# Kernel tuning notes

Measured on AMD Instinct MI355X. Metric: run time of the kernel, lower is better.

## Reference

```python
import jax, jax.numpy as jnp
import numpy as np

NUM_MIXTURES = 10
DIM_INPUT = 512
DIM_FEATURES = 512
SEQ_LEN = 512
BATCH = 16
NUM_CHAR = 1024
DIM_CONTEXT = 256


def setup_inputs() -> dict:
    key = jax.random.key(0)
    ks = jax.random.split(key, 6)
    inputs = jax.random.normal(ks[0], (SEQ_LEN, BATCH, DIM_INPUT), dtype=jnp.float32)
    context_vectors = jax.random.normal(ks[1], (NUM_CHAR, BATCH, DIM_CONTEXT), dtype=jnp.float32)
    init_means = jnp.zeros((BATCH, NUM_MIXTURES), dtype=jnp.float32)
    # StackedLinearLayers params: 2 layers, leaky_relu between, out dim = 3*K
    s1 = 1.0 / np.sqrt(DIM_INPUT)
    s2 = 1.0 / np.sqrt(DIM_FEATURES)
    W1 = jax.random.uniform(ks[2], (DIM_INPUT, DIM_FEATURES), jnp.float32, -s1, s1)
    b1 = jax.random.uniform(ks[3], (DIM_FEATURES,), jnp.float32, -s1, s1)
    W2 = jax.random.uniform(ks[4], (DIM_FEATURES, 3 * NUM_MIXTURES), jnp.float32, -s2, s2)
    b2 = jax.random.uniform(ks[5], (3 * NUM_MIXTURES,), jnp.float32, -s2, s2)
    return dict(inputs=inputs, context_vectors=context_vectors, init_means=init_means,
                W1=W1, b1=b1, W2=W2, b2=b2, extra_chars=0)


def reference(inputs, context_vectors, init_means, W1, b1, W2, b2, extra_chars):
    K = NUM_MIXTURES
    seq_len, batch, _ = inputs.shape
    num_char = context_vectors.shape[0]
    total_char = num_char + extra_chars

    # StackedLinearLayers: leaky_relu MLP, last layer linear -> (S, B, 3K)
    h = jax.nn.leaky_relu(inputs @ W1 + b1, negative_slope=0.01)
    outs = h @ W2 + b2
    outs = jax.nn.softplus(outs)  # pos_fun = softplus

    delta_means, vars_, weights = jnp.split(outs, 3, axis=2)  # each (S, B, K)
    delta_means = delta_means / 25.0
    vars_ = jnp.clip(vars_, 0.01, 100.0)
    means = jnp.cumsum(delta_means, axis=0) + init_means[None, :, :]  # (S, B, K)

    cidxs = jnp.arange(total_char, dtype=jnp.float32)  # (T,)
    # dists: (S, B, K, T)
    dists = -((means[..., None] - cidxs) ** 2) * vars_[..., None]
    # attn_weights = exp(logsumexp over mixtures)
    attn_weights = jnp.exp(
        jax.scipy.special.logsumexp(jnp.log(weights)[..., None] + dists, axis=2)
    )  # (S, B, T)

    # attended contexts: (S, B, D)
    attn_contexts = jnp.einsum('sbc,cbd->sbd', attn_weights[:, :, :num_char], context_vectors)
    return attn_contexts, attn_weights, means, vars_, weights
```

## Files before the change

kernel.cpp:

```cpp
#include <hip/hip_runtime.h>
#include <math.h>

#define S_LEN 512
#define BATCH 16
#define DIN   512
#define DF    512
#define NMIX  10
#define NCHAR 1024
#define DCTX  256
#define M_ROWS (S_LEN*BATCH)

#define OFF_CTXOUT 0
#define OFF_ATTN   (S_LEN*BATCH*DCTX)
#define OFF_MEANS  (OFF_ATTN + S_LEN*BATCH*NCHAR)
#define OFF_VARS   (OFF_MEANS + S_LEN*BATCH*NMIX)
#define OFF_WTS    (OFF_VARS  + S_LEN*BATCH*NMIX)

#define WS_XH    0
#define WS_W1H   (8u<<20)
#define WS_W2T   (9u<<20)
#define WS_HH    (10u<<20)
#define WS_CTXH  (18u<<20)
#define WS_ATTNH (26u<<20)
#define WS_BOUND (44u<<20)

#define NX4     1048576
#define NW14    65536
#define NCTX4   1048576
#define CVT4    (NX4 + NW14 + NCTX4)
#define CVT_BLOCKS (CVT4/256)
#define W2T_BLOCKS 64

typedef float    f32x16 __attribute__((ext_vector_type(16)));
typedef _Float16 f16x8  __attribute__((ext_vector_type(8)));

__device__ __forceinline__ unsigned short f2h(float x) {
    union { _Float16 h; unsigned short u; } cv;
    cv.h = (_Float16)x;
    return cv.u;
}
__device__ __forceinline__ ushort4 cvt4(float4 v) {
    ushort4 o; o.x = f2h(v.x); o.y = f2h(v.y); o.z = f2h(v.z); o.w = f2h(v.w);
    return o;
}

__global__ __launch_bounds__(256) void convert_kernel(
    const float* __restrict__ X, const float* __restrict__ W1,
    const float* __restrict__ ctx, const float* __restrict__ W2,
    unsigned short* __restrict__ Xh, unsigned short* __restrict__ W1h,
    unsigned short* __restrict__ ctxh, float* __restrict__ W2T,
    unsigned int* __restrict__ bound)
{
    const int bid = blockIdx.x;
    if (bid < CVT_BLOCKS) {
        const int i4 = bid*256 + threadIdx.x;
        if (i4 < NX4) {
            ((ushort4*)Xh)[i4] = cvt4(((const float4*)X)[i4]);
        } else if (i4 < NX4 + NW14) {
            ((ushort4*)W1h)[i4 - NX4] = cvt4(((const float4*)W1)[i4 - NX4]);
        } else {
            const int j = i4 - NX4 - NW14;
            ((ushort4*)ctxh)[j] = cvt4(((const float4*)ctx)[j]);
        }
    } else if (bid < CVT_BLOCKS + W2T_BLOCKS) {
        const int idx = (bid - CVT_BLOCKS)*256 + threadIdx.x;
        if (idx < 512*32) {
            const int j = idx >> 9, k = idx & 511;
            W2T[idx] = (j < 30) ? W2[k*30 + j] : 0.f;
        }
    } else {
        if (threadIdx.x < BATCH) bound[threadIdx.x] = 0u;
    }
}

__global__ __launch_bounds__(256) void gemm1_kernel(
    const unsigned short* __restrict__ Xh, const unsigned short* __restrict__ W1h,
    const float* __restrict__ b1, unsigned short* __restrict__ Hh)
{
    __shared__ __align__(16) unsigned short As[64*72];
    __shared__ __align__(16) unsigned short Bs[64*72];
    const int row0 = (blockIdx.x >> 3) * 64;
    const int n0   = (blockIdx.x & 7)  * 64;
    const int tid  = threadIdx.x;
    const int lane = tid & 63, w = tid >> 6;
    const int wr = (w >> 1) * 32, wc = (w & 1) * 32;
    const int m  = lane & 31,  g  = lane >> 5;
    const int sa = tid >> 2,   ka = (tid & 3) * 16;
    const int kb = tid & 63,   wb = tid >> 6;

    f32x16 acc = {};

    for (int kt = 0; kt < DIN; kt += 64) {
        uint4 av0 = *(const uint4*)(Xh  + (size_t)(row0+sa)*DIN + kt + ka);
        uint4 av1 = *(const uint4*)(Xh  + (size_t)(row0+sa)*DIN + kt + ka + 8);
        uint4 bv0 = *(const uint4*)(W1h + (size_t)(kt+kb)*DF + n0 + wb*16);
        uint4 bv1 = *(const uint4*)(W1h + (size_t)(kt+kb)*DF + n0 + wb*16 + 8);
        __syncthreads();
        *(uint4*)(As + sa*72 + ka)     = av0;
        *(uint4*)(As + sa*72 + ka + 8) = av1;
        {
            union { uint4 u; unsigned short s[8]; } p0, p1;
            p0.u = bv0; p1.u = bv1;
            #pragma unroll
            for (int i = 0; i < 8; i++) Bs[(wb*16 + i)*72 + kb]     = p0.s[i];
            #pragma unroll
            for (int i = 0; i < 8; i++) Bs[(wb*16 + 8 + i)*72 + kb] = p1.s[i];
        }
        __syncthreads();
        #pragma unroll
        for (int ks = 0; ks < 64; ks += 16) {
            f16x8 af = *(const f16x8*)(As + (wr+m)*72 + ks + g*8);
            f16x8 bf = *(const f16x8*)(Bs + (wc+m)*72 + ks + g*8);
            acc = __builtin_amdgcn_mfma_f32_32x32x16_f16(af, bf, acc, 0, 0, 0);
        }
    }
    const int ncol = n0 + wc + m;
    const float bb = b1[ncol];
    #pragma unroll
    for (int r = 0; r < 16; r++) {
        const int rowloc = (r & 3) + 8*(r >> 2) + 4*g;
        const int row = row0 + wr + rowloc;
        float v = acc[r] + bb;
        v = v > 0.f ? v : 0.01f * v;
        Hh[(size_t)row*DF + ncol] = f2h(v);
    }
}

__global__ __launch_bounds__(256) void gemm2_kernel(
    const unsigned short* __restrict__ Hh, const float* __restrict__ W2T,
    const float* __restrict__ b2,
    float* __restrict__ dmeans, float* __restrict__ dvars, float* __restrict__ dwts)
{
    __shared__ __align__(16) unsigned short Hs[32*520];
    const int tid = threadIdx.x;
    const int r0  = blockIdx.x * 32;
    {
        const uint4* src = (const uint4*)(Hh + (size_t)r0*DF);
        #pragma unroll
        for (int i = 0; i < 8; i++) {
            int u   = tid + i*256;
            int row = u >> 6;
            int col = (u & 63) * 8;
            *(uint4*)(Hs + row*520 + col) = src[u];
        }
    }
    __syncthreads();

    const int r  = tid & 31;
    const int j0 = tid >> 5;
    const unsigned short* hrow = Hs + r*520;
    float acc[4] = {0.f, 0.f, 0.f, 0.f};

    for (int k0 = 0; k0 < DF; k0 += 8) {
        union { uint4 u; _Float16 h[8]; } hv;
        hv.u = *(const uint4*)(hrow + k0);
        float wv[4][8];
        #pragma unroll
        for (int q = 0; q < 4; q++) {
            *(float4*)(wv[q])     = *(const float4*)(W2T + (size_t)(j0 + q*8)*DF + k0);
            *(float4*)(wv[q] + 4) = *(const float4*)(W2T + (size_t)(j0 + q*8)*DF + k0 + 4);
        }
        #pragma unroll
        for (int i = 0; i < 8; i++) {
            float hf = (float)hv.h[i];
            acc[0] = fmaf(hf, wv[0][i], acc[0]);
            acc[1] = fmaf(hf, wv[1][i], acc[1]);
            acc[2] = fmaf(hf, wv[2][i], acc[2]);
            acc[3] = fmaf(hf, wv[3][i], acc[3]);
        }
    }
    const int row = r0 + r;
    #pragma unroll
    for (int q = 0; q < 4; q++) {
        const int j = j0 + q*8;
        if (j >= 30) continue;
        float dot = acc[q] + b2[j];
        float sp  = fmaxf(dot, 0.f) + log1pf(__expf(-fabsf(dot)));
        if (j < 10)       dmeans[row*NMIX + j]      = sp / 25.0f;
        else if (j < 20)  dvars [row*NMIX + (j-10)] = fminf(fmaxf(sp, 0.01f), 100.f);
        else              dwts  [row*NMIX + (j-20)] = sp;
    }
}

__global__ __launch_bounds__(512) void scan_kernel(
    const float* __restrict__ init_means, float* __restrict__ means,
    const float* __restrict__ vars_g, unsigned int* __restrict__ bound)
{
    const int p    = blockIdx.x;
    const int s    = threadIdx.x;
    const int lane = s & 63;
    const int wid  = s >> 6;

    float x = means[s*(BATCH*NMIX) + p];
    #pragma unroll
    for (int d = 1; d < 64; d <<= 1) {
        float tv = __shfl_up(x, d, 64);
        if (lane >= d) x += tv;
    }
    __shared__ float wsum[8];
    __shared__ float wmax[8];
    if (lane == 63) wsum[wid] = x;
    __syncthreads();
    float off = init_means[p];
    for (int i = 0; i < wid; i++) off += wsum[i];
    x += off;
    means[s*(BATCH*NMIX) + p] = x;

    float v = vars_g[s*(BATCH*NMIX) + p];
    float reach = x + 4.8f * rsqrtf(v);
    #pragma unroll
    for (int d = 32; d >= 1; d >>= 1)
        reach = fmaxf(reach, __shfl_xor(reach, d, 64));
    if (lane == 0) wmax[wid] = reach;
    __syncthreads();
    if (s == 0) {
        float mx = wmax[0];
        #pragma unroll
        for (int i = 1; i < 8; i++) mx = fmaxf(mx, wmax[i]);
        atomicMax((int*)&bound[p / NMIX], __float_as_int(mx));
    }
}

__global__ __launch_bounds__(256) void attn_kernel(
    const float* __restrict__ means, const float* __restrict__ vars,
    const float* __restrict__ wts,   const unsigned int* __restrict__ bound,
    float* __restrict__ attn, unsigned short* __restrict__ attnh)
{
    const int row = blockIdx.x;
    const int b   = row & (BATCH-1);
    const int tid = threadIdx.x;
    const int bd  = (int)__int_as_float((int)bound[b]);
    const int kmax = min(NCHAR, (bd + 64) & ~63);
    const int t0  = tid * 4;

    float o[4] = {0.f, 0.f, 0.f, 0.f};
    if (t0 <= bd) {
        float m[NMIX], v[NMIX], w[NMIX];
        #pragma unroll
        for (int k = 0; k < NMIX; k++) {
            m[k] = means[row*NMIX + k];
            v[k] = vars [row*NMIX + k];
            w[k] = wts  [row*NMIX + k];
        }
        #pragma unroll
        for (int i = 0; i < 4; i++) {
            const float t = (float)(t0 + i);
            float sum = 0.f;
            #pragma unroll
            for (int k = 0; k < NMIX; k++) {
                float d = t - m[k];
                sum += w[k] * __expf(-d*d*v[k]);
            }
            o[i] = sum;
        }
    }
    *(float4*)(attn + (size_t)row*NCHAR + t0) = make_float4(o[0],o[1],o[2],o[3]);
    if (t0 < kmax) {
        ushort4 h; h.x = f2h(o[0]); h.y = f2h(o[1]); h.z = f2h(o[2]); h.w = f2h(o[3]);
        *(ushort4*)(attnh + (size_t)row*NCHAR + t0) = h;
    }
}

__global__ __launch_bounds__(256) void ctx_mfma_kernel(
    const unsigned short* __restrict__ attnh, const unsigned short* __restrict__ ctxh,
    const unsigned int* __restrict__ bound, float* __restrict__ out)
{
    __shared__ __align__(16) unsigned short As[64*72];
    __shared__ __align__(16) unsigned short Bs[64*72];
    const int bid  = blockIdx.x;
    const int b    = bid >> 5;
    const int rem  = bid & 31;
    const int s0   = (rem >> 2) * 64;
    const int d0   = (rem & 3)  * 64;
    const int tid  = threadIdx.x;
    const int lane = tid & 63, w = tid >> 6;
    const int wr = (w >> 1) * 32, wc = (w & 1) * 32;
    const int m  = lane & 31,  g  = lane >> 5;
    const int sl = tid >> 2,   tq = (tid & 3) * 16;
    const int tb = tid & 63,   db = (tid >> 6) * 16;

    const int bd   = (int)__int_as_float((int)bound[b]);
    const int kmax = min(NCHAR, (bd + 64) & ~63);

    f32x16 acc = {};
    const unsigned short* abase = attnh + (size_t)(s0+sl)*(BATCH*NCHAR) + b*NCHAR + tq;
    const unsigned short* bbase = ctxh  + (size_t)b*DCTX + d0 + db;

    for (int kt = 0; kt < kmax; kt += 64) {
        uint4 a0  = *(const uint4*)(abase + kt);
        uint4 a1  = *(const uint4*)(abase + kt + 8);
        uint4 bv0 = *(const uint4*)(bbase + (size_t)(kt+tb)*(BATCH*DCTX));
        uint4 bv1 = *(const uint4*)(bbase + (size_t)(kt+tb)*(BATCH*DCTX) + 8);
        __syncthreads();
        *(uint4*)(As + sl*72 + tq)     = a0;
        *(uint4*)(As + sl*72 + tq + 8) = a1;
        {
            union { uint4 u; unsigned short s[8]; } p0, p1;
            p0.u = bv0; p1.u = bv1;
            #pragma unroll
            for (int i = 0; i < 8; i++) Bs[(db + i)*72 + tb]     = p0.s[i];
            #pragma unroll
            for (int i = 0; i < 8; i++) Bs[(db + 8 + i)*72 + tb] = p1.s[i];
        }
        __syncthreads();
        #pragma unroll
        for (int ks = 0; ks < 64; ks += 16) {
            f16x8 af = *(const f16x8*)(As + (wr+m)*72 + ks + g*8);
            f16x8 bf = *(const f16x8*)(Bs + (wc+m)*72 + ks + g*8);
            acc = __builtin_amdgcn_mfma_f32_32x32x16_f16(af, bf, acc, 0, 0, 0);
        }
    }
    #pragma unroll
    for (int r = 0; r < 16; r++) {
        int rowloc = (r & 3) + 8*(r >> 2) + 4*g;
        int s = s0 + wr + rowloc;
        out[(size_t)s*(BATCH*DCTX) + b*DCTX + d0 + wc + m] = acc[r];
    }
}

extern "C" void kernel_launch(void* const* d_in, const int* in_sizes, int n_in,
                              void* d_out, int out_size, void* d_ws, size_t ws_size,
                              hipStream_t stream)
{
    const float* X     = (const float*)d_in[0];
    const float* ctx   = (const float*)d_in[1];
    const float* initm = (const float*)d_in[2];
    const float* W1    = (const float*)d_in[3];
    const float* b1    = (const float*)d_in[4];
    const float* W2    = (const float*)d_in[5];
    const float* b2    = (const float*)d_in[6];

    float* out      = (float*)d_out;
    float* out_ctx  = out + OFF_CTXOUT;
    float* out_attn = out + OFF_ATTN;
    float* out_mean = out + OFF_MEANS;
    float* out_var  = out + OFF_VARS;
    float* out_wts  = out + OFF_WTS;

    char* ws = (char*)d_ws;
    unsigned short* Xh    = (unsigned short*)(ws + WS_XH);
    unsigned short* W1h   = (unsigned short*)(ws + WS_W1H);
    float*          W2T   = (float*)         (ws + WS_W2T);
    unsigned short* Hh    = (unsigned short*)(ws + WS_HH);
    unsigned short* ctxh  = (unsigned short*)(ws + WS_CTXH);
    unsigned short* attnh = (unsigned short*)(ws + WS_ATTNH);
    unsigned int*   bnd   = (unsigned int*)  (ws + WS_BOUND);

    convert_kernel<<<CVT_BLOCKS + W2T_BLOCKS + 1, 256, 0, stream>>>(
        X, W1, ctx, W2, Xh, W1h, ctxh, W2T, bnd);
    gemm1_kernel<<<(M_ROWS/64)*(DF/64), 256, 0, stream>>>(Xh, W1h, b1, Hh);
    gemm2_kernel<<<M_ROWS/32, 256, 0, stream>>>(Hh, W2T, b2, out_mean, out_var, out_wts);
    scan_kernel<<<BATCH*NMIX, 512, 0, stream>>>(initm, out_mean, out_var, bnd);
    attn_kernel<<<M_ROWS, 256, 0, stream>>>(out_mean, out_var, out_wts, bnd,
                                            out_attn, attnh);
    ctx_mfma_kernel<<<16*8*4, 256, 0, stream>>>(attnh, ctxh, bnd, out_ctx);
}
```

Before: 152.2 us.

## Fuse attention weight computation into context GEMM and pre-transpose W1

Merges the attention-weight kernel into the context MFMA kernel. Each block computes its fp16 attention tile directly into shared memory instead of writing it to a workspace buffer and reading it back, and the dh==0 blocks also write the fp32 attention output, including zeros beyond the bound. The convert kernel now transposes W1 into an n-major fp16 layout so gemm1 can stage B with vector stores instead of scalar scattered LDS writes. In exchange, the exp work is duplicated across the two d-halves, and the fused grid is only 256 blocks, so occupancy may fall.

```diff
diff --git a/kernel.cpp b/kernel.cpp
--- a/kernel.cpp
+++ b/kernel.cpp
@@ -17,18 +17,16 @@
 #define OFF_WTS    (OFF_VARS  + S_LEN*BATCH*NMIX)
 
 #define WS_XH    0
-#define WS_W1H   (8u<<20)
+#define WS_W1T   (8u<<20)
 #define WS_W2T   (9u<<20)
 #define WS_HH    (10u<<20)
 #define WS_CTXH  (18u<<20)
-#define WS_ATTNH (26u<<20)
 #define WS_BOUND (44u<<20)
 
 #define NX4     1048576
-#define NW14    65536
 #define NCTX4   1048576
-#define CVT4    (NX4 + NW14 + NCTX4)
-#define CVT_BLOCKS (CVT4/256)
+#define CVT_BLOCKS ((NX4 + NCTX4)/256)
+#define W1T_BLOCKS 64
 #define W2T_BLOCKS 64
 
 typedef float    f32x16 __attribute__((ext_vector_type(16)));
@@ -47,34 +45,52 @@
 __global__ __launch_bounds__(256) void convert_kernel(
     const float* __restrict__ X, const float* __restrict__ W1,
     const float* __restrict__ ctx, const float* __restrict__ W2,
-    unsigned short* __restrict__ Xh, unsigned short* __restrict__ W1h,
+    unsigned short* __restrict__ Xh, unsigned short* __restrict__ W1T,
     unsigned short* __restrict__ ctxh, float* __restrict__ W2T,
     unsigned int* __restrict__ bound)
 {
     const int bid = blockIdx.x;
+    const int tid = threadIdx.x;
     if (bid < CVT_BLOCKS) {
-        const int i4 = bid*256 + threadIdx.x;
-        if (i4 < NX4) {
-            ((ushort4*)Xh)[i4] = cvt4(((const float4*)X)[i4]);
-        } else if (i4 < NX4 + NW14) {
-            ((ushort4*)W1h)[i4 - NX4] = cvt4(((const float4*)W1)[i4 - NX4]);
-        } else {
-            const int j = i4 - NX4 - NW14;
-            ((ushort4*)ctxh)[j] = cvt4(((const float4*)ctx)[j]);
-        }
-    } else if (bid < CVT_BLOCKS + W2T_BLOCKS) {
-        const int idx = (bid - CVT_BLOCKS)*256 + threadIdx.x;
+        const int i4 = bid*256 + tid;
+        if (i4 < NX4) ((ushort4*)Xh)[i4] = cvt4(((const float4*)X)[i4]);
+        else          ((ushort4*)ctxh)[i4 - NX4] = cvt4(((const float4*)ctx)[i4 - NX4]);
+    } else if (bid < CVT_BLOCKS + W1T_BLOCKS) {
+        __shared__ unsigned short tile[64*68];
+        const int b2 = bid - CVT_BLOCKS;
+        const int k0 = (b2 >> 3) * 64, n0 = (b2 & 7) * 64;
+        #pragma unroll
+        for (int q = 0; q < 4; q++) {
+            const int r = q*16 + (tid >> 4);
+            const int c = (tid & 15) * 4;
+            float4 v = *(const float4*)(W1 + (size_t)(k0+r)*DF + n0 + c);
+            *(ushort4*)(tile + r*68 + c) = cvt4(v);
+        }
+        __syncthreads();
+        #pragma unroll
+        for (int q = 0; q < 4; q++) {
+            const int n  = q*16 + (tid >> 4);
+            const int kq = (tid & 15) * 4;
+            ushort4 o;
+            o.x = tile[(kq+0)*68 + n];
+            o.y = tile[(kq+1)*68 + n];
+            o.z = tile[(kq+2)*68 + n];
+            o.w = tile[(kq+3)*68 + n];
+            *(ushort4*)(W1T + (size_t)(n0+n)*DIN + k0 + kq) = o;
+        }
+    } else if (bid < CVT_BLOCKS + W1T_BLOCKS + W2T_BLOCKS) {
+        const int idx = (bid - CVT_BLOCKS - W1T_BLOCKS)*256 + tid;
         if (idx < 512*32) {
             const int j = idx >> 9, k = idx & 511;
             W2T[idx] = (j < 30) ? W2[k*30 + j] : 0.f;
         }
     } else {
-        if (threadIdx.x < BATCH) bound[threadIdx.x] = 0u;
+        if (tid < BATCH) bound[tid] = 0u;
     }
 }
 
 __global__ __launch_bounds__(256) void gemm1_kernel(
-    const unsigned short* __restrict__ Xh, const unsigned short* __restrict__ W1h,
+    const unsigned short* __restrict__ Xh, const unsigned short* __restrict__ W1T,
     const float* __restrict__ b1, unsigned short* __restrict__ Hh)
 {
     __shared__ __align__(16) unsigned short As[64*72];
@@ -86,26 +102,21 @@
     const int wr = (w >> 1) * 32, wc = (w & 1) * 32;
     const int m  = lane & 31,  g  = lane >> 5;
     const int sa = tid >> 2,   ka = (tid & 3) * 16;
-    const int kb = tid & 63,   wb = tid >> 6;
 
     f32x16 acc = {};
+    const unsigned short* aptr = Xh  + (size_t)(row0+sa)*DIN + ka;
+    const unsigned short* bptr = W1T + (size_t)(n0 +sa)*DIN + ka;
 
     for (int kt = 0; kt < DIN; kt += 64) {
-        uint4 av0 = *(const uint4*)(Xh  + (size_t)(row0+sa)*DIN + kt + ka);
-        uint4 av1 = *(const uint4*)(Xh  + (size_t)(row0+sa)*DIN + kt + ka + 8);
-        uint4 bv0 = *(const uint4*)(W1h + (size_t)(kt+kb)*DF + n0 + wb*16);
-        uint4 bv1 = *(const uint4*)(W1h + (size_t)(kt+kb)*DF + n0 + wb*16 + 8);
+        uint4 av0 = *(const uint4*)(aptr + kt);
+        uint4 av1 = *(const uint4*)(aptr + kt + 8);
+        uint4 bv0 = *(const uint4*)(bptr + kt);
+        uint4 bv1 = *(const uint4*)(bptr + kt + 8);
         __syncthreads();
         *(uint4*)(As + sa*72 + ka)     = av0;
         *(uint4*)(As + sa*72 + ka + 8) = av1;
-        {
-            union { uint4 u; unsigned short s[8]; } p0, p1;
-            p0.u = bv0; p1.u = bv1;
-            #pragma unroll
-            for (int i = 0; i < 8; i++) Bs[(wb*16 + i)*72 + kb]     = p0.s[i];
-            #pragma unroll
-            for (int i = 0; i < 8; i++) Bs[(wb*16 + 8 + i)*72 + kb] = p1.s[i];
-        }
+        *(uint4*)(Bs + sa*72 + ka)     = bv0;
+        *(uint4*)(Bs + sa*72 + ka + 8) = bv1;
         __syncthreads();
         #pragma unroll
         for (int ks = 0; ks < 64; ks += 16) {
@@ -221,100 +232,109 @@
     }
 }
 
-__global__ __launch_bounds__(256) void attn_kernel(
+__global__ __launch_bounds__(256) void attn_ctx_kernel(
     const float* __restrict__ means, const float* __restrict__ vars,
     const float* __restrict__ wts,   const unsigned int* __restrict__ bound,
-    float* __restrict__ attn, unsigned short* __restrict__ attnh)
-{
-    const int row = blockIdx.x;
-    const int b   = row & (BATCH-1);
+    const unsigned short* __restrict__ ctxh,
+    float* __restrict__ attn, float* __restrict__ out)
+{
+    __shared__ __align__(16) unsigned short As[64*72];
+    __shared__ __align__(16) unsigned short Bs[128*72];
+    const int bid = blockIdx.x;
+    const int b   = bid >> 4;
+    const int s0  = ((bid >> 1) & 7) * 64;
+    const int dh  = bid & 1;
     const int tid = threadIdx.x;
-    const int bd  = (int)__int_as_float((int)bound[b]);
-    const int kmax = min(NCHAR, (bd + 64) & ~63);
-    const int t0  = tid * 4;
-
-    float o[4] = {0.f, 0.f, 0.f, 0.f};
-    if (t0 <= bd) {
-        float m[NMIX], v[NMIX], w[NMIX];
-        #pragma unroll
-        for (int k = 0; k < NMIX; k++) {
-            m[k] = means[row*NMIX + k];
-            v[k] = vars [row*NMIX + k];
-            w[k] = wts  [row*NMIX + k];
-        }
-        #pragma unroll
-        for (int i = 0; i < 4; i++) {
-            const float t = (float)(t0 + i);
-            float sum = 0.f;
-            #pragma unroll
-            for (int k = 0; k < NMIX; k++) {
-                float d = t - m[k];
-                sum += w[k] * __expf(-d*d*v[k]);
-            }
-            o[i] = sum;
-        }
-    }
-    *(float4*)(attn + (size_t)row*NCHAR + t0) = make_float4(o[0],o[1],o[2],o[3]);
-    if (t0 < kmax) {
-        ushort4 h; h.x = f2h(o[0]); h.y = f2h(o[1]); h.z = f2h(o[2]); h.w = f2h(o[3]);
-        *(ushort4*)(attnh + (size_t)row*NCHAR + t0) = h;
-    }
-}
-
-__global__ __launch_bounds__(256) void ctx_mfma_kernel(
-    const unsigned short* __restrict__ attnh, const unsigned short* __restrict__ ctxh,
-    const unsigned int* __restrict__ bound, float* __restrict__ out)
-{
-    __shared__ __align__(16) unsigned short As[64*72];
-    __shared__ __align__(16) unsigned short Bs[64*72];
-    const int bid  = blockIdx.x;
-    const int b    = bid >> 5;
-    const int rem  = bid & 31;
-    const int s0   = (rem >> 2) * 64;
-    const int d0   = (rem & 3)  * 64;
-    const int tid  = threadIdx.x;
-    const int lane = tid & 63, w = tid >> 6;
-    const int wr = (w >> 1) * 32, wc = (w & 1) * 32;
-    const int m  = lane & 31,  g  = lane >> 5;
-    const int sl = tid >> 2,   tq = (tid & 3) * 16;
-    const int tb = tid & 63,   db = (tid >> 6) * 16;
 
     const int bd   = (int)__int_as_float((int)bound[b]);
     const int kmax = min(NCHAR, (bd + 64) & ~63);
 
-    f32x16 acc = {};
-    const unsigned short* abase = attnh + (size_t)(s0+sl)*(BATCH*NCHAR) + b*NCHAR + tq;
-    const unsigned short* bbase = ctxh  + (size_t)b*DCTX + d0 + db;
+    const int sA = tid >> 2;
+    const int tq = tid & 3;
+    const int row = (s0 + sA)*BATCH + b;
+    float m[NMIX], v[NMIX], w[NMIX];
+    #pragma unroll
+    for (int k = 0; k < NMIX; k++) {
+        m[k] = means[row*NMIX + k];
+        v[k] = vars [row*NMIX + k];
+        w[k] = wts  [row*NMIX + k];
+    }
+
+    const int lane = tid & 63, wv_ = tid >> 6;
+    const int m_ = lane & 31, g = lane >> 5;
+    const int wc = wv_ * 32;
+    const int tb = tid & 63, dgrp = (tid >> 6) * 32;
+    const unsigned short* bbase = ctxh + (size_t)b*DCTX + dh*128 + dgrp;
+
+    f32x16 acc0 = {}, acc1 = {};
 
     for (int kt = 0; kt < kmax; kt += 64) {
-        uint4 a0  = *(const uint4*)(abase + kt);
-        uint4 a1  = *(const uint4*)(abase + kt + 8);
-        uint4 bv0 = *(const uint4*)(bbase + (size_t)(kt+tb)*(BATCH*DCTX));
-        uint4 bv1 = *(const uint4*)(bbase + (size_t)(kt+tb)*(BATCH*DCTX) + 8);
-        __syncthreads();
-        *(uint4*)(As + sl*72 + tq)     = a0;
-        *(uint4*)(As + sl*72 + tq + 8) = a1;
-        {
-            union { uint4 u; unsigned short s[8]; } p0, p1;
-            p0.u = bv0; p1.u = bv1;
+        const int tbase = kt + tq*16;
+        float o[16];
+        #pragma unroll
+        for (int i = 0; i < 16; i++) o[i] = 0.f;
+        if (tbase <= bd) {
             #pragma unroll
-            for (int i = 0; i < 8; i++) Bs[(db + i)*72 + tb]     = p0.s[i];
+            for (int i = 0; i < 16; i++) {
+                const float t = (float)(tbase + i);
+                float sum = 0.f;
+                #pragma unroll
+                for (int k = 0; k < NMIX; k++) {
+                    float d = t - m[k];
+                    sum += w[k] * __expf(-d*d*v[k]);
+                }
+                o[i] = sum;
+            }
+        }
+        if (dh == 0) {
+            float* ap = attn + (size_t)row*NCHAR + tbase;
             #pragma unroll
-            for (int i = 0; i < 8; i++) Bs[(db + 8 + i)*72 + tb] = p1.s[i];
+            for (int i = 0; i < 4; i++)
+                *(float4*)(ap + i*4) = make_float4(o[i*4],o[i*4+1],o[i*4+2],o[i*4+3]);
+        }
+        uint4 bv[4];
+        #pragma unroll
+        for (int q = 0; q < 4; q++)
+            bv[q] = *(const uint4*)(bbase + (size_t)(kt+tb)*(BATCH*DCTX) + q*8);
+        __syncthreads();
+        #pragma unroll
+        for (int i = 0; i < 4; i++) {
+            ushort4 h;
+            h.x = f2h(o[i*4]); h.y = f2h(o[i*4+1]); h.z = f2h(o[i*4+2]); h.w = f2h(o[i*4+3]);
+            *(ushort4*)(As + sA*72 + tq*16 + i*4) = h;
+        }
+        #pragma unroll
+        for (int q = 0; q < 4; q++) {
+            union { uint4 u; unsigned short s[8]; } p;
+            p.u = bv[q];
+            #pragma unroll
+            for (int i = 0; i < 8; i++)
+                Bs[(dgrp + q*8 + i)*72 + tb] = p.s[i];
         }
         __syncthreads();
         #pragma unroll
         for (int ks = 0; ks < 64; ks += 16) {
-            f16x8 af = *(const f16x8*)(As + (wr+m)*72 + ks + g*8);
-            f16x8 bf = *(const f16x8*)(Bs + (wc+m)*72 + ks + g*8);
-            acc = __builtin_amdgcn_mfma_f32_32x32x16_f16(af, bf, acc, 0, 0, 0);
-        }
-    }
+            f16x8 a0 = *(const f16x8*)(As + (m_)*72      + ks + g*8);
+            f16x8 a1 = *(const f16x8*)(As + (32 + m_)*72 + ks + g*8);
+            f16x8 bf = *(const f16x8*)(Bs + (wc + m_)*72 + ks + g*8);
+            acc0 = __builtin_amdgcn_mfma_f32_32x32x16_f16(a0, bf, acc0, 0, 0, 0);
+            acc1 = __builtin_amdgcn_mfma_f32_32x32x16_f16(a1, bf, acc1, 0, 0, 0);
+        }
+    }
+    if (dh == 0) {
+        const float4 z = make_float4(0.f,0.f,0.f,0.f);
+        for (int kt = kmax; kt < NCHAR; kt += 64) {
+            float* ap = attn + (size_t)row*NCHAR + kt + tq*16;
+            #pragma unroll
+            for (int i = 0; i < 4; i++) *(float4*)(ap + i*4) = z;
+        }
+    }
+    const int dglob = dh*128 + wc + m_;
     #pragma unroll
     for (int r = 0; r < 16; r++) {
-        int rowloc = (r & 3) + 8*(r >> 2) + 4*g;
-        int s = s0 + wr + rowloc;
-        out[(size_t)s*(BATCH*DCTX) + b*DCTX + d0 + wc + m] = acc[r];
+        const int rowloc = (r & 3) + 8*(r >> 2) + 4*g;
+        out[(size_t)(s0 + rowloc)*(BATCH*DCTX) + b*DCTX + dglob]      = acc0[r];
+        out[(size_t)(s0 + 32 + rowloc)*(BATCH*DCTX) + b*DCTX + dglob] = acc1[r];
     }
 }
 
@@ -339,19 +359,17 @@
 
     char* ws = (char*)d_ws;
     unsigned short* Xh    = (unsigned short*)(ws + WS_XH);
-    unsigned short* W1h   = (unsigned short*)(ws + WS_W1H);
+    unsigned short* W1T   = (unsigned short*)(ws + WS_W1T);
     float*          W2T   = (float*)         (ws + WS_W2T);
     unsigned short* Hh    = (unsigned short*)(ws + WS_HH);
     unsigned short* ctxh  = (unsigned short*)(ws + WS_CTXH);
-    unsigned short* attnh = (unsigned short*)(ws + WS_ATTNH);
     unsigned int*   bnd   = (unsigned int*)  (ws + WS_BOUND);
 
-    convert_kernel<<<CVT_BLOCKS + W2T_BLOCKS + 1, 256, 0, stream>>>(
-        X, W1, ctx, W2, Xh, W1h, ctxh, W2T, bnd);
-    gemm1_kernel<<<(M_ROWS/64)*(DF/64), 256, 0, stream>>>(Xh, W1h, b1, Hh);
+    convert_kernel<<<CVT_BLOCKS + W1T_BLOCKS + W2T_BLOCKS + 1, 256, 0, stream>>>(
+        X, W1, ctx, W2, Xh, W1T, ctxh, W2T, bnd);
+    gemm1_kernel<<<(M_ROWS/64)*(DF/64), 256, 0, stream>>>(Xh, W1T, b1, Hh);
     gemm2_kernel<<<M_ROWS/32, 256, 0, stream>>>(Hh, W2T, b2, out_mean, out_var, out_wts);
     scan_kernel<<<BATCH*NMIX, 512, 0, stream>>>(initm, out_mean, out_var, bnd);
-    attn_kernel<<<M_ROWS, 256, 0, stream>>>(out_mean, out_var, out_wts, bnd,
-                                            out_attn, attnh);
-    ctx_mfma_kernel<<<16*8*4, 256, 0, stream>>>(attnh, ctxh, bnd, out_ctx);
-}
+    attn_ctx_kernel<<<BATCH*8*2, 256, 0, stream>>>(out_mean, out_var, out_wts, bnd,
+                                                   ctxh, out_attn, out_ctx);
+}
```

New measurement: 207.1 us. 36.1% more time.
